# Performance work log

Hardware: AMD Instinct MI355X
Metric: run time of the kernel (lower is better)

## Reference

```python
import jax, jax.numpy as jnp
import numpy as np

EMBED = 1024
HEADS = 16
HEAD_DIM = EMBED // HEADS
OUT_DIM = 1024


def setup_inputs() -> dict:
    key = jax.random.key(0)
    ks = jax.random.split(key, 8)
    N, L = 2, 2048
    values = jax.random.normal(ks[0], (N, L, EMBED), dtype=jnp.float32)
    keys_t = jax.random.normal(ks[1], (N, L, EMBED), dtype=jnp.float32)
    query = jax.random.normal(ks[2], (N, L, EMBED), dtype=jnp.float32)
    s = 1.0 / np.sqrt(HEAD_DIM)
    Wv = jax.random.normal(ks[3], (HEAD_DIM, HEAD_DIM), dtype=jnp.float32) * s
    Wk = jax.random.normal(ks[4], (HEAD_DIM, HEAD_DIM), dtype=jnp.float32) * s
    Wq = jax.random.normal(ks[5], (HEAD_DIM, HEAD_DIM), dtype=jnp.float32) * s
    Wout = jax.random.normal(ks[6], (OUT_DIM, EMBED), dtype=jnp.float32) * (1.0 / np.sqrt(EMBED))
    bout = jax.random.normal(ks[7], (OUT_DIM,), dtype=jnp.float32) * 0.01
    return {"values": values, "keys": keys_t, "query": query,
            "Wv": Wv, "Wk": Wk, "Wq": Wq, "Wout": Wout, "bout": bout}


def reference(values, keys, query, Wv, Wk, Wq, Wout, bout):
    N, Lq, _ = query.shape
    Lk = keys.shape[1]
    # split into heads: (N, L, H, D)
    v = values.reshape(N, Lk, HEADS, HEAD_DIM)
    k = keys.reshape(N, Lk, HEADS, HEAD_DIM)
    q = query.reshape(N, Lq, HEADS, HEAD_DIM)
    # per-head shared linear projections (torch Linear: x @ W.T, no bias)
    v = jnp.einsum('nlhd,ed->nlhe', v, Wv)
    k = jnp.einsum('nlhd,ed->nlhe', k, Wk)
    q = jnp.einsum('nqhd,ed->nqhe', q, Wq)
    # scores (N, H, Q, K); NOTE: scale is 1/sqrt(embed_size), per original code
    scores = jnp.einsum('nqhd,nkhd->nhqk', q, k) / jnp.sqrt(jnp.float32(EMBED))
    attn = jax.nn.softmax(scores, axis=-1)
    out = jnp.einsum('nhqk,nkhd->nqhd', attn, v).reshape(N, Lq, EMBED)
    # fc_out: x @ Wout.T + bout
    return out @ Wout.T + bout
```

## Files before the change

kernel.cpp:

```cpp
#include <hip/hip_runtime.h>
#include <cstdint>

typedef __attribute__((ext_vector_type(8))) short short8;
typedef __attribute__((ext_vector_type(4))) float floatx4;
typedef __attribute__((ext_vector_type(16))) float floatx16;
typedef __attribute__((ext_vector_type(8))) _Float16 half8;

#define DEV __device__ __forceinline__

constexpr int NB = 2, Lseq = 2048, NH = 16, HD = 64, EMB = 1024;
constexpr float QSCALE = 0.03125f * 1.4426950408889634f;

DEV uint32_t pack2(float lo, float hi) {
  uint32_t a = __builtin_bit_cast(uint32_t, lo) + 0x8000u;
  uint32_t b = __builtin_bit_cast(uint32_t, hi) + 0x8000u;
  return __builtin_amdgcn_perm(b, a, 0x07060302);
}

DEV uint32_t packh2(float lo, float hi) {
  return __builtin_bit_cast(uint32_t, __builtin_amdgcn_cvt_pkrtz(lo, hi));
}

DEV void gl_lds16(const void* g, void* l) {
  __builtin_amdgcn_global_load_lds((const __attribute__((address_space(1))) void*)g,
                                   (__attribute__((address_space(3))) void*)l, 16, 0, 0);
}

DEV void pl32(uint32_t& x, uint32_t& y) {
  typedef __attribute__((ext_vector_type(2))) unsigned int uint2v;
  uint2v r = __builtin_amdgcn_permlane32_swap(x, y, false, false);
  x = r[0];
  y = r[1];
}

DEV short8 ld8bf(const float* p, float sc) {
  float4 u = *(const float4*)p;
  float4 v = *(const float4*)(p + 4);
  union { short8 s; uint32_t d[4]; } r;
  r.d[0] = pack2(u.x * sc, u.y * sc);
  r.d[1] = pack2(u.z * sc, u.w * sc);
  r.d[2] = pack2(v.x * sc, v.y * sc);
  r.d[3] = pack2(v.z * sc, v.w * sc);
  return r.s;
}

__global__ __launch_bounds__(256) void prep_kernel(
    const float* __restrict__ values, const float* __restrict__ keysrc,
    const float* __restrict__ query, const float* __restrict__ Wv,
    const float* __restrict__ Wk, const float* __restrict__ Wq,
    const float* __restrict__ Wout,
    uint16_t* __restrict__ qp, uint16_t* __restrict__ kp,
    uint16_t* __restrict__ vp, uint16_t* __restrict__ wbf) {
  const int t = threadIdx.x, w = t >> 6, lane = t & 63;
  const int quad = lane >> 4, l16 = lane & 15;
  const int wid = blockIdx.x * 4 + w;
  const int mat = wid >> 10, sub = wid & 1023;

  if (mat == 3) {
#pragma unroll
    for (int i = 0; i < 4; ++i) {
      int idx = sub * 256 + i * 64 + lane;
      float4 v = ((const float4*)Wout)[idx];
      uint2 p;
      p.x = pack2(v.x, v.y);
      p.y = pack2(v.z, v.w);
      ((uint2*)wbf)[idx] = p;
    }
    return;
  }

  floatx4 c[4][4];
#pragma unroll
  for (int i = 0; i < 4; ++i)
#pragma unroll
    for (int j = 0; j < 4; ++j) c[i][j] = floatx4{0.f, 0.f, 0.f, 0.f};

  if (mat < 2) {
    const float* src = mat ? keysrc : query;
    const float* W   = mat ? Wk : Wq;
    const float asc  = mat ? 1.f : QSCALE;
    uint16_t* dst    = mat ? kp : qp;
    const int R0 = sub * 64;
    short8 a[4][2], b[4][2];
#pragma unroll
    for (int dc = 0; dc < 2; ++dc) {
#pragma unroll
      for (int f = 0; f < 4; ++f) {
        a[f][dc] = ld8bf(W + (size_t)(f * 16 + l16) * 64 + dc * 32 + quad * 8, asc);
        b[f][dc] = ld8bf(src + (size_t)(R0 + f * 16 + l16) * 64 + dc * 32 + quad * 8, 1.f);
      }
    }
#pragma unroll
    for (int dc = 0; dc < 2; ++dc)
#pragma unroll
      for (int mf = 0; mf < 4; ++mf)
#pragma unroll
        for (int nf = 0; nf < 4; ++nf)
          c[mf][nf] = __builtin_amdgcn_mfma_f32_16x16x32_bf16(a[mf][dc], b[nf][dc], c[mf][nf], 0, 0, 0);
#pragma unroll
    for (int nf = 0; nf < 4; ++nf) {
      int r = R0 + nf * 16 + l16;
      int h = r & 15, l = (r >> 4) & 2047, n = r >> 15;
      uint16_t* drow = dst + ((size_t)(n * 16 + h) * 2048 + l) * 64;
#pragma unroll
      for (int mf = 0; mf < 4; ++mf) {
        uint2 pk;
        pk.x = pack2(c[mf][nf][0], c[mf][nf][1]);
        pk.y = pack2(c[mf][nf][2], c[mf][nf][3]);
        *(uint2*)(drow + mf * 16 + quad * 4) = pk;
      }
    }
  } else {
    const int nh = sub >> 5, L0 = (sub & 31) * 64;
    const int n = nh >> 4, h = nh & 15;
    short8 a[4][2], b[4][2];
#pragma unroll
    for (int dc = 0; dc < 2; ++dc) {
#pragma unroll
      for (int f = 0; f < 4; ++f) {
        a[f][dc] = ld8bf(values + (size_t)(n * 2048 + L0 + f * 16 + l16) * 1024 + h * 64 + dc * 32 + quad * 8, 1.f);
        b[f][dc] = ld8bf(Wv + (size_t)(f * 16 + l16) * 64 + dc * 32 + quad * 8, 1.f);
      }
    }
#pragma unroll
    for (int dc = 0; dc < 2; ++dc)
#pragma unroll
      for (int mf = 0; mf < 4; ++mf)
#pragma unroll
        for (int nf = 0; nf < 4; ++nf)
          c[mf][nf] = __builtin_amdgcn_mfma_f32_16x16x32_bf16(a[mf][dc], b[nf][dc], c[mf][nf], 0, 0, 0);
#pragma unroll
    for (int nf = 0; nf < 4; ++nf) {
      int d = nf * 16 + l16;
      uint16_t* drow = vp + ((size_t)nh * 64 + d) * 2048 + L0;
#pragma unroll
      for (int mf = 0; mf < 4; ++mf) {
        uint2 pk;
        pk.x = packh2(c[mf][nf][0], c[mf][nf][1]);
        pk.y = packh2(c[mf][nf][2], c[mf][nf][3]);
        *(uint2*)(drow + mf * 16 + quad * 4) = pk;
      }
    }
  }
}

__global__ __launch_bounds__(256, 4) void flash_kernel(const uint16_t* __restrict__ qp,
                                                       const uint16_t* __restrict__ kp,
                                                       const uint16_t* __restrict__ vp,
                                                       uint32_t* __restrict__ opart,
                                                       float* __restrict__ psum) {
  constexpr int kbn = 16;
  __shared__ uint16_t Kt[2][64 * 64];
  __shared__ uint16_t Vt[2][64 * 64];
  const int t = threadIdx.x;
  const int w = t >> 6, lane = t & 63, hi = lane >> 5, l32 = lane & 31;
  const int nh = blockIdx.x, qt = blockIdx.y, kh = blockIdx.z;
  const int q0w = qt * 128 + w * 32;
  const uint16_t* Qb = qp + (size_t)nh * Lseq * HD;
  const uint16_t* Kb = kp + (size_t)nh * Lseq * HD + (size_t)kh * 1024 * 64;
  const uint16_t* Vb = vp + (size_t)nh * HD * Lseq;
  const int vcol0 = kh * 1024;
  const int srow = lane >> 3, sc8 = (lane & 7) ^ (lane >> 3);

  short8 bq[4];
#pragma unroll
  for (int dc = 0; dc < 4; ++dc)
    bq[dc] = *(const short8*)(Qb + (size_t)(q0w + l32) * 64 + dc * 16 + hi * 8);

  floatx16 o[2];
  float lsum = 0.f;
#pragma unroll
  for (int r = 0; r < 16; ++r) { o[0][r] = 0.f; o[1][r] = 0.f; }

  auto stage = [&](int tile, int buf) {
#pragma unroll
    for (int i = 0; i < 2; ++i) {
      int r0 = w * 16 + i * 8;
      int sc = sc8 ^ ((w * 2 + i) & 3);
      gl_lds16(Kb + (size_t)tile * 4096 + (r0 + srow) * 64 + sc * 8, &Kt[buf][r0 * 64]);
      gl_lds16(Vb + (size_t)(r0 + srow) * Lseq + vcol0 + tile * 64 + sc * 8, &Vt[buf][r0 * 64]);
    }
  };

  stage(0, 0);

  for (int kb = 0; kb < kbn; ++kb) {
    __syncthreads();
    const int cur = kb & 1;
    if (kb + 1 < kbn) stage(kb + 1, cur ^ 1);

#pragma unroll
    for (int kt = 0; kt < 2; ++kt) {
      floatx16 s;
#pragma unroll
      for (int r = 0; r < 16; ++r) s[r] = 0.f;
      const int krow = kt * 32 + l32;
      const int ksw = (krow & 7) ^ ((krow >> 3) & 3);
      __builtin_amdgcn_s_setprio(1);
#pragma unroll
      for (int dc = 0; dc < 4; ++dc) {
        short8 ak = *(const short8*)(&Kt[cur][krow * 64 + (((dc << 1) | hi) ^ ksw) * 8]);
        s = __builtin_amdgcn_mfma_f32_32x32x16_bf16(ak, bq[dc], s, 0, 0, 0);
      }
      __builtin_amdgcn_s_setprio(0);

      float ex[16];
#pragma unroll
      for (int r = 0; r < 16; ++r) ex[r] = __builtin_amdgcn_exp2f(s[r]);
      float t0 = (ex[0] + ex[1]) + (ex[2] + ex[3]);
      float t1 = (ex[4] + ex[5]) + (ex[6] + ex[7]);
      float t2 = (ex[8] + ex[9]) + (ex[10] + ex[11]);
      float t3 = (ex[12] + ex[13]) + (ex[14] + ex[15]);
      lsum += (t0 + t1) + (t2 + t3);

      uint32_t a0 = packh2(ex[0], ex[1]);
      uint32_t a1 = packh2(ex[2], ex[3]);
      uint32_t b0 = packh2(ex[4], ex[5]);
      uint32_t b1 = packh2(ex[6], ex[7]);
      uint32_t c0 = packh2(ex[8], ex[9]);
      uint32_t c1 = packh2(ex[10], ex[11]);
      uint32_t d0 = packh2(ex[12], ex[13]);
      uint32_t d1 = packh2(ex[14], ex[15]);
      pl32(a0, b0); pl32(a1, b1); pl32(c0, d0); pl32(c1, d1);
      union { half8 h; uint32_t u[4]; } f0, f1;
      f0.u[0] = a0; f0.u[1] = a1; f0.u[2] = b0; f0.u[3] = b1;
      f1.u[0] = c0; f1.u[1] = c1; f1.u[2] = d0; f1.u[3] = d1;

      __builtin_amdgcn_s_setprio(1);
#pragma unroll
      for (int dt = 0; dt < 2; ++dt) {
        const int vrow = dt * 32 + l32;
        const int vsw = (vrow & 7) ^ ((vrow >> 3) & 3);
        half8 av0 = *(const half8*)(&Vt[cur][vrow * 64 + ((kt * 4 + hi) ^ vsw) * 8]);
        o[dt] = __builtin_amdgcn_mfma_f32_32x32x16_f16(av0, f0.h, o[dt], 0, 0, 0);
        half8 av1 = *(const half8*)(&Vt[cur][vrow * 64 + ((kt * 4 + 2 + hi) ^ vsw) * 8]);
        o[dt] = __builtin_amdgcn_mfma_f32_32x32x16_f16(av1, f1.h, o[dt], 0, 0, 0);
      }
      __builtin_amdgcn_s_setprio(0);
    }
  }

  {
    uint32_t sx = __builtin_bit_cast(uint32_t, lsum), sy = sx;
    pl32(sx, sy);
    float oth = __builtin_bit_cast(float, (lane < 32) ? sy : sx);
    lsum += oth;
  }

  uint32_t* ob = opart + ((size_t)(((nh * 16 + qt) * 2 + kh) * 4 + w)) * 1024 + lane;
#pragma unroll
  for (int dt = 0; dt < 2; ++dt)
#pragma unroll
    for (int j = 0; j < 8; ++j)
      ob[(dt * 8 + j) * 64] = packh2(o[dt][2 * j], o[dt][2 * j + 1]);
  if (hi == 0)
    psum[((size_t)((nh * 16 + qt) * 2 + kh)) * 128 + w * 32 + l32] = lsum;
}

__global__ __launch_bounds__(256) void combine_kernel(const uint32_t* __restrict__ opart,
                                                      const float* __restrict__ psum,
                                                      uint16_t* __restrict__ xg) {
  __shared__ uint32_t Xs[128 * 32];
  const int t = threadIdx.x, w = t >> 6, lane = t & 63;
  const int hi = lane >> 5, l32 = lane & 31;
  const int nh = blockIdx.x, qt = blockIdx.y;
  const size_t tb0 = (size_t)((nh * 16 + qt) * 2);
  const uint32_t* pa0 = opart + (tb0 * 4 + w) * 1024 + lane;
  const uint32_t* pa1 = opart + ((tb0 + 1) * 4 + w) * 1024 + lane;
  const float l0 = psum[tb0 * 128 + w * 32 + l32];
  const float l1 = psum[(tb0 + 1) * 128 + w * 32 + l32];
  const float inv = __builtin_amdgcn_rcpf(l0 + l1);
  const int ql = w * 32 + l32;

#pragma unroll
  for (int k = 0; k < 16; ++k) {
    const int dt = k >> 3, j = k & 7;
    union { uint32_t u; _Float16 h[2]; } u0, u1;
    u0.u = pa0[k * 64];
    u1.u = pa1[k * 64];
    float v0 = ((float)u0.h[0] + (float)u1.h[0]) * inv;
    float v1 = ((float)u0.h[1] + (float)u1.h[1]) * inv;
    const int d = dt * 32 + (j >> 1) * 8 + (j & 1) * 2 + 4 * hi;
    Xs[ql * 32 + ((d >> 1) ^ ((ql & 7) << 2))] = pack2(v0, v1);
  }
  __syncthreads();

  const int nn = nh >> 4, h = nh & 15;
#pragma unroll
  for (int pass = 0; pass < 2; ++pass) {
    int row = pass * 64 + (t >> 2), l4 = t & 3;
    uint4 v = *(const uint4*)(&Xs[row * 32 + ((l4 * 8) ^ ((row & 7) << 2))]);
    uint4 v2 = *(const uint4*)(&Xs[row * 32 + (((l4 * 8 + 4)) ^ ((row & 7) << 2))]);
    uint16_t* xr = xg + ((size_t)(nn * 2048 + qt * 128 + row)) * 1024 + h * 64 + l4 * 16;
    *(uint4*)xr = v;
    *(uint4*)(xr + 8) = v2;
  }
}

__global__ __launch_bounds__(256, 2) void out_gemm(const uint16_t* __restrict__ Xg,
                                                   const uint16_t* __restrict__ Wb,
                                                   const float* __restrict__ bias,
                                                   float* __restrict__ out) {
  __shared__ uint16_t Xt[3][64 * 64];
  __shared__ uint16_t Wt[3][128 * 64];
  const int t = threadIdx.x, w = t >> 6, lane = t & 63, quad = lane >> 4, l16 = lane & 15;
  const int m0 = blockIdx.x * 64, o0 = blockIdx.y * 128;
  const int srow = lane >> 3, sc8 = (lane & 7) ^ (lane >> 3);

  floatx4 acc[8];
#pragma unroll
  for (int j = 0; j < 8; ++j) acc[j] = floatx4{0.f, 0.f, 0.f, 0.f};

  auto stage = [&](int buf, int kt) {
#pragma unroll
    for (int i = 0; i < 2; ++i) {
      int r0 = w * 16 + i * 8;
      gl_lds16(Xg + (size_t)(m0 + r0 + srow) * 1024 + kt * 64 + sc8 * 8, &Xt[buf][r0 * 64]);
    }
#pragma unroll
    for (int i = 0; i < 4; ++i) {
      int r0 = w * 32 + i * 8;
      gl_lds16(Wb + (size_t)(o0 + r0 + srow) * 1024 + kt * 64 + sc8 * 8, &Wt[buf][r0 * 64]);
    }
  };

  stage(0, 0);
  stage(1, 1);

  int cur = 0;
  for (int kt = 0; kt < 16; ++kt) {
    if (kt + 1 < 16) asm volatile("s_waitcnt vmcnt(6)" ::: "memory");
    else             asm volatile("s_waitcnt vmcnt(0)" ::: "memory");
    __builtin_amdgcn_s_barrier();
    if (kt + 2 < 16) {
      int tgt = cur + 2; if (tgt >= 3) tgt -= 3;
      stage(tgt, kt + 2);
    }
#pragma unroll
    for (int kc = 0; kc < 2; ++kc) {
      int ra = w * 16 + l16;
      short8 a = *(const short8*)(&Xt[cur][ra * 64 + ((kc * 4 + quad) ^ (ra & 7)) * 8]);
#pragma unroll
      for (int nf = 0; nf < 8; ++nf) {
        int rb = nf * 16 + l16;
        short8 b = *(const short8*)(&Wt[cur][rb * 64 + ((kc * 4 + quad) ^ (rb & 7)) * 8]);
        acc[nf] = __builtin_amdgcn_mfma_f32_16x16x32_bf16(a, b, acc[nf], 0, 0, 0);
      }
    }
    asm volatile("s_waitcnt lgkmcnt(0)" ::: "memory");
    cur = (cur + 1 == 3) ? 0 : cur + 1;
  }

#pragma unroll
  for (int nf = 0; nf < 8; ++nf) {
    float bv = bias[o0 + nf * 16 + l16];
#pragma unroll
    for (int r = 0; r < 4; ++r)
      out[(size_t)(m0 + w * 16 + quad * 4 + r) * 1024 + o0 + nf * 16 + l16] = acc[nf][r] + bv;
  }
}

extern "C" void kernel_launch(void* const* d_in, const int* in_sizes, int n_in,
                              void* d_out, int out_size, void* d_ws, size_t ws_size,
                              hipStream_t stream) {
  const float* values = (const float*)d_in[0];
  const float* keys   = (const float*)d_in[1];
  const float* query  = (const float*)d_in[2];
  const float* Wv     = (const float*)d_in[3];
  const float* Wk     = (const float*)d_in[4];
  const float* Wq     = (const float*)d_in[5];
  const float* Wout   = (const float*)d_in[6];
  const float* bout   = (const float*)d_in[7];
  float* out = (float*)d_out;
  (void)ws_size;

  uint16_t* ws  = (uint16_t*)d_ws;
  uint16_t* qp  = ws;
  uint16_t* kp  = ws + (size_t)4194304;
  uint16_t* vp  = ws + (size_t)8388608;
  uint16_t* wbf = ws + (size_t)12582912;
  uint32_t* opart = (uint32_t*)(ws + (size_t)13631488);
  float* psum = (float*)(ws + (size_t)22020096);
  uint16_t* xp  = ws + (size_t)22282240;

  prep_kernel<<<dim3(1024), dim3(256), 0, stream>>>(values, keys, query, Wv, Wk, Wq, Wout,
                                                    qp, kp, vp, wbf);
  flash_kernel<<<dim3(32, 16, 2), dim3(256), 0, stream>>>(qp, kp, vp, opart, psum);
  combine_kernel<<<dim3(32, 16), dim3(256), 0, stream>>>(opart, psum, xp);
  out_gemm<<<dim3(64, 8), dim3(256), 0, stream>>>(xp, wbf, bout, out);
}
```

Baseline: 173.2 us.

## Fuse split-K combine into flash kernel using 512-thread blocks with LDS reduction

The two key-halves of each query tile are now handled by two groups of four waves inside one 512-thread block instead of two separate blocks. After the main loop, the second half writes its partial output and row sums to shared memory, and the first half adds them, normalizes, and writes bf16 directly to the fc_out input. This removes the separate combine kernel launch and the global round trip of fp16 partials and sums. The cost is doubled shared memory per block, a coarser grid of fewer, larger blocks, and half the waves sitting idle during the final merge.

After: 170.0 us. No clear change (-1.8%).

```diff
diff --git a/kernel.cpp b/kernel.cpp
--- a/kernel.cpp
+++ b/kernel.cpp
@@ -144,18 +144,18 @@
   }
 }
 
-__global__ __launch_bounds__(256, 4) void flash_kernel(const uint16_t* __restrict__ qp,
+__global__ __launch_bounds__(512, 2) void flash_kernel(const uint16_t* __restrict__ qp,
                                                        const uint16_t* __restrict__ kp,
                                                        const uint16_t* __restrict__ vp,
-                                                       uint32_t* __restrict__ opart,
-                                                       float* __restrict__ psum) {
+                                                       uint16_t* __restrict__ xg) {
   constexpr int kbn = 16;
-  __shared__ uint16_t Kt[2][64 * 64];
-  __shared__ uint16_t Vt[2][64 * 64];
+  __shared__ uint16_t Kt[2][2][64 * 64];
+  __shared__ uint16_t Vt[2][2][64 * 64];
   const int t = threadIdx.x;
   const int w = t >> 6, lane = t & 63, hi = lane >> 5, l32 = lane & 31;
-  const int nh = blockIdx.x, qt = blockIdx.y, kh = blockIdx.z;
-  const int q0w = qt * 128 + w * 32;
+  const int kh = w >> 2, wq = w & 3;
+  const int nh = blockIdx.x, qt = blockIdx.y;
+  const int q0w = qt * 128 + wq * 32;
   const uint16_t* Qb = qp + (size_t)nh * Lseq * HD;
   const uint16_t* Kb = kp + (size_t)nh * Lseq * HD + (size_t)kh * 1024 * 64;
   const uint16_t* Vb = vp + (size_t)nh * HD * Lseq;
@@ -175,10 +175,10 @@
   auto stage = [&](int tile, int buf) {
 #pragma unroll
     for (int i = 0; i < 2; ++i) {
-      int r0 = w * 16 + i * 8;
-      int sc = sc8 ^ ((w * 2 + i) & 3);
-      gl_lds16(Kb + (size_t)tile * 4096 + (r0 + srow) * 64 + sc * 8, &Kt[buf][r0 * 64]);
-      gl_lds16(Vb + (size_t)(r0 + srow) * Lseq + vcol0 + tile * 64 + sc * 8, &Vt[buf][r0 * 64]);
+      int r0 = wq * 16 + i * 8;
+      int sc = sc8 ^ ((wq * 2 + i) & 3);
+      gl_lds16(Kb + (size_t)tile * 4096 + (r0 + srow) * 64 + sc * 8, &Kt[kh][buf][r0 * 64]);
+      gl_lds16(Vb + (size_t)(r0 + srow) * Lseq + vcol0 + tile * 64 + sc * 8, &Vt[kh][buf][r0 * 64]);
     }
   };
 
@@ -199,7 +199,7 @@
       __builtin_amdgcn_s_setprio(1);
 #pragma unroll
       for (int dc = 0; dc < 4; ++dc) {
-        short8 ak = *(const short8*)(&Kt[cur][krow * 64 + (((dc << 1) | hi) ^ ksw) * 8]);
+        short8 ak = *(const short8*)(&Kt[kh][cur][krow * 64 + (((dc << 1) | hi) ^ ksw) * 8]);
         s = __builtin_amdgcn_mfma_f32_32x32x16_bf16(ak, bq[dc], s, 0, 0, 0);
       }
       __builtin_amdgcn_s_setprio(0);
@@ -231,9 +231,9 @@
       for (int dt = 0; dt < 2; ++dt) {
         const int vrow = dt * 32 + l32;
         const int vsw = (vrow & 7) ^ ((vrow >> 3) & 3);
-        half8 av0 = *(const half8*)(&Vt[cur][vrow * 64 + ((kt * 4 + hi) ^ vsw) * 8]);
+        half8 av0 = *(const half8*)(&Vt[kh][cur][vrow * 64 + ((kt * 4 + hi) ^ vsw) * 8]);
         o[dt] = __builtin_amdgcn_mfma_f32_32x32x16_f16(av0, f0.h, o[dt], 0, 0, 0);
-        half8 av1 = *(const half8*)(&Vt[cur][vrow * 64 + ((kt * 4 + 2 + hi) ^ vsw) * 8]);
+        half8 av1 = *(const half8*)(&Vt[kh][cur][vrow * 64 + ((kt * 4 + 2 + hi) ^ vsw) * 8]);
         o[dt] = __builtin_amdgcn_mfma_f32_32x32x16_f16(av1, f1.h, o[dt], 0, 0, 0);
       }
       __builtin_amdgcn_s_setprio(0);
@@ -247,53 +247,39 @@
     lsum += oth;
   }
 
-  uint32_t* ob = opart + ((size_t)(((nh * 16 + qt) * 2 + kh) * 4 + w)) * 1024 + lane;
-#pragma unroll
-  for (int dt = 0; dt < 2; ++dt)
-#pragma unroll
-    for (int j = 0; j < 8; ++j)
-      ob[(dt * 8 + j) * 64] = packh2(o[dt][2 * j], o[dt][2 * j + 1]);
-  if (hi == 0)
-    psum[((size_t)((nh * 16 + qt) * 2 + kh)) * 128 + w * 32 + l32] = lsum;
-}
-
-__global__ __launch_bounds__(256) void combine_kernel(const uint32_t* __restrict__ opart,
-                                                      const float* __restrict__ psum,
-                                                      uint16_t* __restrict__ xg) {
-  __shared__ uint32_t Xs[128 * 32];
-  const int t = threadIdx.x, w = t >> 6, lane = t & 63;
-  const int hi = lane >> 5, l32 = lane & 31;
-  const int nh = blockIdx.x, qt = blockIdx.y;
-  const size_t tb0 = (size_t)((nh * 16 + qt) * 2);
-  const uint32_t* pa0 = opart + (tb0 * 4 + w) * 1024 + lane;
-  const uint32_t* pa1 = opart + ((tb0 + 1) * 4 + w) * 1024 + lane;
-  const float l0 = psum[tb0 * 128 + w * 32 + l32];
-  const float l1 = psum[(tb0 + 1) * 128 + w * 32 + l32];
-  const float inv = __builtin_amdgcn_rcpf(l0 + l1);
-  const int ql = w * 32 + l32;
-
-#pragma unroll
-  for (int k = 0; k < 16; ++k) {
-    const int dt = k >> 3, j = k & 7;
-    union { uint32_t u; _Float16 h[2]; } u0, u1;
-    u0.u = pa0[k * 64];
-    u1.u = pa1[k * 64];
-    float v0 = ((float)u0.h[0] + (float)u1.h[0]) * inv;
-    float v1 = ((float)u0.h[1] + (float)u1.h[1]) * inv;
-    const int d = dt * 32 + (j >> 1) * 8 + (j & 1) * 2 + 4 * hi;
-    Xs[ql * 32 + ((d >> 1) ^ ((ql & 7) << 2))] = pack2(v0, v1);
-  }
+  uint32_t* scr = (uint32_t*)&Kt[0][0][0];
+  float* lscr = (float*)&Vt[0][0][0];
   __syncthreads();
-
-  const int nn = nh >> 4, h = nh & 15;
-#pragma unroll
-  for (int pass = 0; pass < 2; ++pass) {
-    int row = pass * 64 + (t >> 2), l4 = t & 3;
-    uint4 v = *(const uint4*)(&Xs[row * 32 + ((l4 * 8) ^ ((row & 7) << 2))]);
-    uint4 v2 = *(const uint4*)(&Xs[row * 32 + (((l4 * 8 + 4)) ^ ((row & 7) << 2))]);
-    uint16_t* xr = xg + ((size_t)(nn * 2048 + qt * 128 + row)) * 1024 + h * 64 + l4 * 16;
-    *(uint4*)xr = v;
-    *(uint4*)(xr + 8) = v2;
+  if (kh == 1) {
+#pragma unroll
+    for (int dt = 0; dt < 2; ++dt)
+#pragma unroll
+      for (int j = 0; j < 8; ++j)
+        scr[(dt * 8 + j) * 256 + wq * 64 + lane] = packh2(o[dt][2 * j], o[dt][2 * j + 1]);
+    if (hi == 0) lscr[wq * 32 + l32] = lsum;
+  }
+  __syncthreads();
+  if (kh == 0) {
+    const float l1 = lscr[wq * 32 + l32];
+    const float inv = __builtin_amdgcn_rcpf(lsum + l1);
+    const int nn = nh >> 4, h = nh & 15;
+    uint16_t* xr = xg + ((size_t)(nn * 2048 + q0w + l32)) * 1024 + h * 64;
+#pragma unroll
+    for (int dt = 0; dt < 2; ++dt)
+#pragma unroll
+      for (int rg = 0; rg < 4; ++rg) {
+        union { uint32_t u; _Float16 hh[2]; } u0, u1;
+        u0.u = scr[(dt * 8 + rg * 2) * 256 + wq * 64 + lane];
+        u1.u = scr[(dt * 8 + rg * 2 + 1) * 256 + wq * 64 + lane];
+        float s0 = o[dt][rg * 4 + 0] + (float)u0.hh[0];
+        float s1 = o[dt][rg * 4 + 1] + (float)u0.hh[1];
+        float s2 = o[dt][rg * 4 + 2] + (float)u1.hh[0];
+        float s3 = o[dt][rg * 4 + 3] + (float)u1.hh[1];
+        uint2 pk;
+        pk.x = pack2(s0 * inv, s1 * inv);
+        pk.y = pack2(s2 * inv, s3 * inv);
+        *(uint2*)(xr + dt * 32 + rg * 8 + 4 * hi) = pk;
+      }
   }
 }
 
@@ -379,13 +365,10 @@
   uint16_t* kp  = ws + (size_t)4194304;
   uint16_t* vp  = ws + (size_t)8388608;
   uint16_t* wbf = ws + (size_t)12582912;
-  uint32_t* opart = (uint32_t*)(ws + (size_t)13631488);
-  float* psum = (float*)(ws + (size_t)22020096);
-  uint16_t* xp  = ws + (size_t)22282240;
+  uint16_t* xp  = ws + (size_t)13631488;
 
   prep_kernel<<<dim3(1024), dim3(256), 0, stream>>>(values, keys, query, Wv, Wk, Wq, Wout,
                                                     qp, kp, vp, wbf);
-  flash_kernel<<<dim3(32, 16, 2), dim3(256), 0, stream>>>(qp, kp, vp, opart, psum);
-  combine_kernel<<<dim3(32, 16), dim3(256), 0, stream>>>(opart, psum, xp);
+  flash_kernel<<<dim3(32, 16), dim3(512), 0, stream>>>(qp, kp, vp, xp);
   out_gemm<<<dim3(64, 8), dim3(256), 0, stream>>>(xp, wbf, bout, out);
 }
```
